# Kernel tuning notes

Hardware: AMD Instinct MI355X
Metric: run time of the kernel (lower is better)

The kernel has to match this reference:

```python
import jax, jax.numpy as jnp
import numpy as np

S, E, K = 100000, 30000, 1000
D, F = 64, 128
B = 16384
NNZ_S, NNZ_E, NNZ_K = 1600000, 480000, 32000
LAYERS = 3
MOMENTUM = 0.9
LEAK = 0.1


def setup_inputs() -> dict:
    key = jax.random.key(0)
    ks = jax.random.split(key, 24)
    inp = {}
    inp['student_id'] = jax.random.randint(ks[0], (B,), 0, S, dtype=jnp.int32)
    inp['exercise_id'] = jax.random.randint(ks[1], (B,), 0, E, dtype=jnp.int32)
    inp['q_mask'] = jnp.ones((B, K), jnp.float32)
    # embedding tables (xavier-ish scale)
    inp['stu_emb'] = jax.random.normal(ks[2], (S, D), jnp.float32) * 0.05
    inp['exer_emb'] = jax.random.normal(ks[3], (E, D), jnp.float32) * 0.05
    inp['know_emb'] = jax.random.normal(ks[4], (K, D), jnp.float32) * 0.05
    inp['impact_emb'] = jax.random.normal(ks[5], (E, D), jnp.float32) * 0.05
    # sparse adjacencies in COO form (rows, cols, vals); vals ~ normalized weights
    inp['s_rows'] = jax.random.randint(ks[6], (NNZ_S,), 0, S, dtype=jnp.int32)
    inp['s_cols'] = jax.random.randint(ks[7], (NNZ_S,), 0, S, dtype=jnp.int32)
    inp['s_vals'] = jax.random.uniform(ks[8], (NNZ_S,), jnp.float32) / 16.0
    inp['e_rows'] = jax.random.randint(ks[9], (NNZ_E,), 0, E, dtype=jnp.int32)
    inp['e_cols'] = jax.random.randint(ks[10], (NNZ_E,), 0, E, dtype=jnp.int32)
    inp['e_vals'] = jax.random.uniform(ks[11], (NNZ_E,), jnp.float32) / 16.0
    inp['k_rows'] = jax.random.randint(ks[12], (NNZ_K,), 0, K, dtype=jnp.int32)
    inp['k_cols'] = jax.random.randint(ks[13], (NNZ_K,), 0, K, dtype=jnp.int32)
    inp['k_vals'] = jax.random.uniform(ks[14], (NNZ_K,), jnp.float32) / 32.0
    # linear layers (stored as [in, out])
    inp['W_stu'] = jax.random.normal(ks[15], (D, F), jnp.float32) * 0.1
    inp['b_stu'] = jnp.zeros((F,), jnp.float32)
    inp['W_exer'] = jax.random.normal(ks[16], (D, F), jnp.float32) * 0.1
    inp['b_exer'] = jnp.zeros((F,), jnp.float32)
    inp['W_know'] = jax.random.normal(ks[17], (D, F), jnp.float32) * 0.1
    inp['b_know'] = jnp.zeros((F,), jnp.float32)
    inp['W_disc'] = jax.random.normal(ks[18], (D, 1), jnp.float32) * 0.1
    inp['b_disc'] = jnp.zeros((1,), jnp.float32)
    return inp


def spmm(rows, cols, vals, x, n):
    # sparse [n,n] @ dense [n,d] via gather + segment_sum
    return jax.ops.segment_sum(vals[:, None] * x[cols], rows, num_segments=n)


def convolution(emb, rows, cols, vals, n):
    # layers of SpMM with momentum residual; mean over all (layers+1) outputs
    acc = emb
    cur = emb
    for _ in range(LAYERS):
        cur = spmm(rows, cols, vals, cur, n) + MOMENTUM * cur
        acc = acc + cur
    return acc / (LAYERS + 1)


def reference(student_id, exercise_id, q_mask, stu_emb, exer_emb, know_emb,
              impact_emb, s_rows, s_cols, s_vals, e_rows, e_cols, e_vals,
              k_rows, k_cols, k_vals, W_stu, b_stu, W_exer, b_exer,
              W_know, b_know, W_disc, b_disc):
    stu_fwd = convolution(stu_emb, s_rows, s_cols, s_vals, S)    # [S, D]
    exer_fwd = convolution(exer_emb, e_rows, e_cols, e_vals, E)  # [E, D]
    know_fwd = convolution(know_emb, k_rows, k_cols, k_vals, K)  # [K, D]

    batch_student = stu_fwd[student_id]    # [B, D]
    batch_exercise = exer_fwd[exercise_id]  # [B, D]

    student_ts = jax.nn.leaky_relu(batch_student @ W_stu + b_stu, LEAK)   # [B, F]
    diff_ts = jax.nn.leaky_relu(batch_exercise @ W_exer + b_exer, LEAK)  # [B, F]
    knowledge_ts = jax.nn.leaky_relu(know_fwd @ W_know + b_know, LEAK)   # [K, F]
    disc_ts = jax.nn.sigmoid(batch_exercise @ W_disc + b_disc)          # [B, 1]

    student_ts = student_ts @ knowledge_ts.T  # [B, K]
    diff_ts = diff_ts @ knowledge_ts.T        # [B, K]
    knowledge_impact_ts = impact_emb[exercise_id]  # [B, D]
    return (student_ts, diff_ts, disc_ts, knowledge_ts, knowledge_impact_ts)
```

## Files before the change

### kernel.cpp

```cpp
#include <hip/hip_runtime.h>
#include <hip/hip_bf16.h>

#define S_N 100000
#define E_N 30000
#define K_N 1000
#define D_K 64
#define F_K 128
#define B_N 16384
#define NNZ_S 1600000
#define NNZ_E 480000
#define NNZ_K 32000
#define NNZ_TOT (NNZ_S + NNZ_E + NNZ_K)

#define CH_S 49
#define CH_E 15
#define CH_K 1
#define CH_TOT (CH_S + CH_E + CH_K)

#define NB_S 782
#define NB_E 235
#define NB_K 8
#define NB_TOT (NB_S + NB_E + NB_K)

#define CHUNK 4096
#define SB_S 391
#define SB_E 118
#define SB_K 8
#define SB_TOT (SB_S + SB_E + SB_K)

typedef __attribute__((ext_vector_type(8))) short sh8;
typedef __attribute__((ext_vector_type(4))) float f4;

__device__ inline float b2f(ushort u) { return __uint_as_float((unsigned)u << 16); }
__device__ inline ushort f2b(float f) {
    unsigned u = __float_as_uint(f);
    return (ushort)((u + 0x7fffu + ((u >> 16) & 1u)) >> 16);
}

__global__ void count_kernel(const int* __restrict__ sr, const int* __restrict__ er,
                             const int* __restrict__ kr,
                             int* cnt_s, int* cnt_e, int* cnt_k) {
    int i = blockIdx.x * 256 + threadIdx.x;
    if (i >= NNZ_TOT) return;
    if (i < NNZ_S) atomicAdd(&cnt_s[sr[i]], 1);
    else if (i < NNZ_S + NNZ_E) atomicAdd(&cnt_e[er[i - NNZ_S]], 1);
    else atomicAdd(&cnt_k[kr[i - NNZ_S - NNZ_E]], 1);
}

__device__ inline void seg_map(int b, const int* cnt_s, const int* cnt_e, const int* cnt_k,
                               const int** src, int* len, int* chunk, int* seg) {
    if (b < CH_S)            { *src = cnt_s; *len = S_N; *chunk = b;            *seg = 0; }
    else if (b < CH_S + CH_E){ *src = cnt_e; *len = E_N; *chunk = b - CH_S;     *seg = 1; }
    else                     { *src = cnt_k; *len = K_N; *chunk = 0;            *seg = 2; }
}

__global__ void scan_a(const int* cnt_s, const int* cnt_e, const int* cnt_k, int* partials) {
    const int* src; int len, chunk, seg;
    seg_map(blockIdx.x, cnt_s, cnt_e, cnt_k, &src, &len, &chunk, &seg);
    int base = chunk * 2048 + threadIdx.x * 8;
    int s = 0;
    for (int j = 0; j < 8; j++) { int idx = base + j; if (idx < len) s += src[idx]; }
    __shared__ int red[256];
    red[threadIdx.x] = s; __syncthreads();
    for (int off = 128; off > 0; off >>= 1) {
        if (threadIdx.x < off) red[threadIdx.x] += red[threadIdx.x + off];
        __syncthreads();
    }
    if (threadIdx.x == 0) partials[blockIdx.x] = red[0];
}

__global__ void scan_b(const int* partials, int* chunk_off, int* rp_s, int* rp_e, int* rp_k) {
    if (threadIdx.x == 0 && blockIdx.x == 0) {
        int acc = 0;
        for (int i = 0; i < CH_S; i++) { chunk_off[i] = acc; acc += partials[i]; }
        rp_s[S_N] = acc;
        acc = 0;
        for (int i = CH_S; i < CH_S + CH_E; i++) { chunk_off[i] = acc; acc += partials[i]; }
        rp_e[E_N] = acc;
        chunk_off[CH_S + CH_E] = 0;
        rp_k[K_N] = partials[CH_S + CH_E];
    }
}

__global__ void scan_c(const int* cnt_s, const int* cnt_e, const int* cnt_k,
                       const int* chunk_off,
                       int* rp_s, int* rp_e, int* rp_k) {
    const int* src; int len, chunk, seg;
    seg_map(blockIdx.x, cnt_s, cnt_e, cnt_k, &src, &len, &chunk, &seg);
    int* rp = (seg == 0) ? rp_s : (seg == 1) ? rp_e : rp_k;
    int t = threadIdx.x;
    int base = chunk * 2048 + t * 8;
    int v[8]; int s = 0;
    for (int j = 0; j < 8; j++) { int idx = base + j; v[j] = (idx < len) ? src[idx] : 0; s += v[j]; }
    __shared__ int sd[256];
    sd[t] = s; __syncthreads();
    for (int off = 1; off < 256; off <<= 1) {
        int x = (t >= off) ? sd[t - off] : 0;
        __syncthreads();
        sd[t] += x;
        __syncthreads();
    }
    int pre = sd[t] - s + chunk_off[blockIdx.x];
    for (int j = 0; j < 8; j++) {
        int idx = base + j;
        if (idx < len) { rp[idx] = pre; pre += v[j]; }
    }
}

__global__ void stage1_bin(const int* __restrict__ sr, const int* __restrict__ sc,
                           const float* __restrict__ sv,
                           const int* __restrict__ er, const int* __restrict__ ec,
                           const float* __restrict__ ev,
                           const int* __restrict__ kr, const int* __restrict__ kc,
                           const float* __restrict__ kv,
                           const int* __restrict__ rp_s, const int* __restrict__ rp_e,
                           const int* __restrict__ rp_k,
                           int* bcnt, int2* stg_s, int2* stg_e, int2* stg_k) {
    int blk = blockIdx.x;
    const int* rows; const int* cols; const float* vals; const int* rp;
    int2* stg; int boff, nnz, nb, lblk;
    if (blk < SB_S) {
        lblk = blk; rows = sr; cols = sc; vals = sv; rp = rp_s; stg = stg_s;
        boff = 0; nnz = NNZ_S; nb = NB_S;
    } else if (blk < SB_S + SB_E) {
        lblk = blk - SB_S; rows = er; cols = ec; vals = ev; rp = rp_e; stg = stg_e;
        boff = NB_S; nnz = NNZ_E; nb = NB_E;
    } else {
        lblk = blk - SB_S - SB_E; rows = kr; cols = kc; vals = kv; rp = rp_k; stg = stg_k;
        boff = NB_S + NB_E; nnz = NNZ_K; nb = NB_K;
    }
    __shared__ int hist[NB_S];
    __shared__ int wbase[NB_S];
    int t = threadIdx.x;
    for (int i = t; i < nb; i += 256) hist[i] = 0;
    __syncthreads();
    int start = lblk * CHUNK, end = min(start + CHUNK, nnz);
    for (int i = start + t; i < end; i += 256) atomicAdd(&hist[rows[i] >> 7], 1);
    __syncthreads();
    for (int i = t; i < nb; i += 256) {
        int h = hist[i];
        int b0 = h ? atomicAdd(&bcnt[boff + i], h) : 0;
        wbase[i] = rp[i << 7] + b0;
        hist[i] = 0;
    }
    __syncthreads();
    for (int i = start + t; i < end; i += 256) {
        int r = rows[i]; int b = r >> 7;
        int p = wbase[b] + atomicAdd(&hist[b], 1);
        stg[p] = make_int2(((r & 127) << 25) | cols[i], __float_as_int(vals[i]));
    }
}

__global__ void stage2_place(const int* __restrict__ rp_s, const int2* __restrict__ stg_s,
                             int2* pr_s,
                             const int* __restrict__ rp_e, const int2* __restrict__ stg_e,
                             int2* pr_e,
                             const int* __restrict__ rp_k, const int2* __restrict__ stg_k,
                             int2* pr_k) {
    int b = blockIdx.x;
    const int* rp; const int2* stg; int2* pr; int len;
    if (b < NB_S) { rp = rp_s; stg = stg_s; pr = pr_s; len = S_N; }
    else if (b < NB_S + NB_E) { b -= NB_S; rp = rp_e; stg = stg_e; pr = pr_e; len = E_N; }
    else { b -= NB_S + NB_E; rp = rp_k; stg = stg_k; pr = pr_k; len = K_N; }
    int r0 = b << 7;
    int rows = min(128, len - r0);
    __shared__ int nx[128];
    int t = threadIdx.x;
    if (t < rows) nx[t] = rp[r0 + t];
    __syncthreads();
    int j0 = rp[r0], j1 = rp[r0 + rows];
    for (int j = j0 + t; j < j1; j += 256) {
        int2 e = stg[j];
        int r_rel = ((unsigned)e.x) >> 25;
        int col = e.x & 0x01FFFFFF;
        int p = atomicAdd(&nx[r_rel], 1);
        pr[p] = make_int2(col, e.y);
    }
}

__global__ void convert_bf16(const float* __restrict__ a, const float* __restrict__ b,
                             const float* __restrict__ c,
                             ushort* oa, ushort* ob, ushort* oc) {
    const int NA = S_N * 64, NB = E_N * 64, NC = K_N * 64;
    int i = (blockIdx.x * 256 + threadIdx.x) * 4;
    const float* src; ushort* dst;
    if (i < NA) { src = a; dst = oa; }
    else if (i < NA + NB) { i -= NA; src = b; dst = ob; }
    else if (i < NA + NB + NC) { i -= NA + NB; src = c; dst = oc; }
    else return;
    float4 v = *(const float4*)&src[i];
    ushort4 o;
    o.x = f2b(v.x); o.y = f2b(v.y); o.z = f2b(v.z); o.w = f2b(v.w);
    *(ushort4*)&dst[i] = o;
}

__device__ __forceinline__ void spmm_row_compute(
        const int* __restrict__ rp, const int2* __restrict__ pr,
        const ushort* __restrict__ x, int r, int l, float* a) {
    const ushort4* __restrict__ X4 = (const ushort4*)x;
    int j0 = rp[r], j1 = rp[r + 1];
    ushort4 self = X4[r * 16 + l];
    float a0 = 0.9f * b2f(self.x), a1 = 0.9f * b2f(self.y);
    float a2 = 0.9f * b2f(self.z), a3 = 0.9f * b2f(self.w);
    int j = j0;
    for (; j + 8 <= j1; j += 8) {
        int2 q0 = pr[j + 0], q1 = pr[j + 1], q2 = pr[j + 2], q3 = pr[j + 3];
        int2 q4 = pr[j + 4], q5 = pr[j + 5], q6 = pr[j + 6], q7 = pr[j + 7];
        ushort4 v0 = X4[q0.x * 16 + l];
        ushort4 v1 = X4[q1.x * 16 + l];
        ushort4 v2 = X4[q2.x * 16 + l];
        ushort4 v3 = X4[q3.x * 16 + l];
        ushort4 v4 = X4[q4.x * 16 + l];
        ushort4 v5 = X4[q5.x * 16 + l];
        ushort4 v6 = X4[q6.x * 16 + l];
        ushort4 v7 = X4[q7.x * 16 + l];
        float w0 = __int_as_float(q0.y), w1 = __int_as_float(q1.y);
        float w2 = __int_as_float(q2.y), w3 = __int_as_float(q3.y);
        float w4 = __int_as_float(q4.y), w5 = __int_as_float(q5.y);
        float w6 = __int_as_float(q6.y), w7 = __int_as_float(q7.y);
        a0 = fmaf(w0, b2f(v0.x), a0); a1 = fmaf(w0, b2f(v0.y), a1);
        a2 = fmaf(w0, b2f(v0.z), a2); a3 = fmaf(w0, b2f(v0.w), a3);
        a0 = fmaf(w1, b2f(v1.x), a0); a1 = fmaf(w1, b2f(v1.y), a1);
        a2 = fmaf(w1, b2f(v1.z), a2); a3 = fmaf(w1, b2f(v1.w), a3);
        a0 = fmaf(w2, b2f(v2.x), a0); a1 = fmaf(w2, b2f(v2.y), a1);
        a2 = fmaf(w2, b2f(v2.z), a2); a3 = fmaf(w2, b2f(v2.w), a3);
        a0 = fmaf(w3, b2f(v3.x), a0); a1 = fmaf(w3, b2f(v3.y), a1);
        a2 = fmaf(w3, b2f(v3.z), a2); a3 = fmaf(w3, b2f(v3.w), a3);
        a0 = fmaf(w4, b2f(v4.x), a0); a1 = fmaf(w4, b2f(v4.y), a1);
        a2 = fmaf(w4, b2f(v4.z), a2); a3 = fmaf(w4, b2f(v4.w), a3);
        a0 = fmaf(w5, b2f(v5.x), a0); a1 = fmaf(w5, b2f(v5.y), a1);
        a2 = fmaf(w5, b2f(v5.z), a2); a3 = fmaf(w5, b2f(v5.w), a3);
        a0 = fmaf(w6, b2f(v6.x), a0); a1 = fmaf(w6, b2f(v6.y), a1);
        a2 = fmaf(w6, b2f(v6.z), a2); a3 = fmaf(w6, b2f(v6.w), a3);
        a0 = fmaf(w7, b2f(v7.x), a0); a1 = fmaf(w7, b2f(v7.y), a1);
        a2 = fmaf(w7, b2f(v7.z), a2); a3 = fmaf(w7, b2f(v7.w), a3);
    }
    if (j + 4 <= j1) {
        int2 q0 = pr[j + 0], q1 = pr[j + 1], q2 = pr[j + 2], q3 = pr[j + 3];
        ushort4 v0 = X4[q0.x * 16 + l];
        ushort4 v1 = X4[q1.x * 16 + l];
        ushort4 v2 = X4[q2.x * 16 + l];
        ushort4 v3 = X4[q3.x * 16 + l];
        float w0 = __int_as_float(q0.y), w1 = __int_as_float(q1.y);
        float w2 = __int_as_float(q2.y), w3 = __int_as_float(q3.y);
        a0 = fmaf(w0, b2f(v0.x), a0); a1 = fmaf(w0, b2f(v0.y), a1);
        a2 = fmaf(w0, b2f(v0.z), a2); a3 = fmaf(w0, b2f(v0.w), a3);
        a0 = fmaf(w1, b2f(v1.x), a0); a1 = fmaf(w1, b2f(v1.y), a1);
        a2 = fmaf(w1, b2f(v1.z), a2); a3 = fmaf(w1, b2f(v1.w), a3);
        a0 = fmaf(w2, b2f(v2.x), a0); a1 = fmaf(w2, b2f(v2.y), a1);
        a2 = fmaf(w2, b2f(v2.z), a2); a3 = fmaf(w2, b2f(v2.w), a3);
        a0 = fmaf(w3, b2f(v3.x), a0); a1 = fmaf(w3, b2f(v3.y), a1);
        a2 = fmaf(w3, b2f(v3.z), a2); a3 = fmaf(w3, b2f(v3.w), a3);
        j += 4;
    }
    if (j < j1) {
        int last = j1 - 1;
        int2 q0 = pr[j];
        int2 q1 = pr[min(j + 1, last)];
        int2 q2 = pr[min(j + 2, last)];
        int2 q3 = pr[min(j + 3, last)];
        ushort4 v0 = X4[q0.x * 16 + l];
        ushort4 v1 = X4[q1.x * 16 + l];
        ushort4 v2 = X4[q2.x * 16 + l];
        ushort4 v3 = X4[q3.x * 16 + l];
        float w0 = __int_as_float(q0.y);
        float w1 = (j + 1 <= last) ? __int_as_float(q1.y) : 0.f;
        float w2 = (j + 2 <= last) ? __int_as_float(q2.y) : 0.f;
        float w3 = (j + 3 <= last) ? __int_as_float(q3.y) : 0.f;
        a0 = fmaf(w0, b2f(v0.x), a0); a1 = fmaf(w0, b2f(v0.y), a1);
        a2 = fmaf(w0, b2f(v0.z), a2); a3 = fmaf(w0, b2f(v0.w), a3);
        a0 = fmaf(w1, b2f(v1.x), a0); a1 = fmaf(w1, b2f(v1.y), a1);
        a2 = fmaf(w1, b2f(v1.z), a2); a3 = fmaf(w1, b2f(v1.w), a3);
        a0 = fmaf(w2, b2f(v2.x), a0); a1 = fmaf(w2, b2f(v2.y), a1);
        a2 = fmaf(w2, b2f(v2.z), a2); a3 = fmaf(w2, b2f(v2.w), a3);
        a0 = fmaf(w3, b2f(v3.x), a0); a1 = fmaf(w3, b2f(v3.y), a1);
        a2 = fmaf(w3, b2f(v3.z), a2); a3 = fmaf(w3, b2f(v3.w), a3);
    }
    a[0] = a0; a[1] = a1; a[2] = a2; a[3] = a3;
}

__global__ void spmm_full(const int* __restrict__ rp_s, const int2* __restrict__ pr_s,
                          const ushort* __restrict__ xs, ushort* ys,
                          const int* __restrict__ rp_e, const int2* __restrict__ pr_e,
                          const ushort* __restrict__ xe, ushort* ye,
                          const int* __restrict__ rp_k, const int2* __restrict__ pr_k,
                          const ushort* __restrict__ xk, ushort* yk) {
    int w = (blockIdx.x * 256 + threadIdx.x) >> 4;
    int l = threadIdx.x & 15;
    const int* rp; const int2* pr; const ushort* x; ushort* y; int r;
    if (w < S_N) { rp = rp_s; pr = pr_s; x = xs; y = ys; r = w; }
    else if (w < S_N + E_N) { rp = rp_e; pr = pr_e; x = xe; y = ye; r = w - S_N; }
    else if (w < S_N + E_N + K_N) { rp = rp_k; pr = pr_k; x = xk; y = yk; r = w - S_N - E_N; }
    else return;
    float a[4];
    spmm_row_compute(rp, pr, x, r, l, a);
    ushort4 o;
    o.x = f2b(a[0]); o.y = f2b(a[1]); o.z = f2b(a[2]); o.w = f2b(a[3]);
    *(ushort4*)&y[r * 64 + l * 4] = o;
}

__global__ void spmm_last(const int* __restrict__ sid, const int* __restrict__ eid,
                          const int* __restrict__ rp_s, const int2* __restrict__ pr_s,
                          const ushort* __restrict__ xs, ushort* c3s,
                          const int* __restrict__ rp_e, const int2* __restrict__ pr_e,
                          const ushort* __restrict__ xe, ushort* c3e,
                          const int* __restrict__ rp_k, const int2* __restrict__ pr_k,
                          const ushort* __restrict__ xk, ushort* yk) {
    int w = (blockIdx.x * 256 + threadIdx.x) >> 4;
    int l = threadIdx.x & 15;
    const int* rp; const int2* pr; const ushort* x; ushort* y; int r; int orow;
    if (w < B_N) { rp = rp_s; pr = pr_s; x = xs; y = c3s; r = sid[w]; orow = w; }
    else if (w < 2 * B_N) {
        int b = w - B_N;
        rp = rp_e; pr = pr_e; x = xe; y = c3e; r = eid[b]; orow = b;
    } else if (w < 2 * B_N + K_N) {
        r = w - 2 * B_N;
        rp = rp_k; pr = pr_k; x = xk; y = yk; orow = r;
    } else return;
    float a[4];
    spmm_row_compute(rp, pr, x, r, l, a);
    ushort4 o;
    o.x = f2b(a[0]); o.y = f2b(a[1]); o.z = f2b(a[2]); o.w = f2b(a[3]);
    *(ushort4*)&y[orow * 64 + l * 4] = o;
}

__global__ void gather_init(const int* __restrict__ sid, const int* __restrict__ eid,
                            const float* __restrict__ src_s, const float* __restrict__ src_e,
                            const float* __restrict__ src_k,
                            float* bacc_s, float* bacc_e, float* kacc) {
    int i = blockIdx.x * 256 + threadIdx.x;
    const int BD = B_N * 64;
    if (i < BD) {
        int b = i >> 6, d = i & 63;
        bacc_s[i] = src_s[(long)sid[b] * 64 + d];
    } else if (i < 2 * BD) {
        int ii = i - BD; int b = ii >> 6, d = ii & 63;
        bacc_e[ii] = src_e[(long)eid[b] * 64 + d];
    } else if (i < 2 * BD + K_N * 64) {
        int ii = i - 2 * BD;
        kacc[ii] = src_k[ii];
    }
}

__global__ void gather_accb(const int* __restrict__ sid, const int* __restrict__ eid,
                            const ushort* __restrict__ src_s, const ushort* __restrict__ src_e,
                            const ushort* __restrict__ src_k,
                            float* bacc_s, float* bacc_e, float* kacc) {
    int i = blockIdx.x * 256 + threadIdx.x;
    const int BD = B_N * 64;
    if (i < BD) {
        int b = i >> 6, d = i & 63;
        bacc_s[i] += b2f(src_s[(long)sid[b] * 64 + d]);
    } else if (i < 2 * BD) {
        int ii = i - BD; int b = ii >> 6, d = ii & 63;
        bacc_e[ii] += b2f(src_e[(long)eid[b] * 64 + d]);
    } else if (i < 2 * BD + K_N * 64) {
        int ii = i - 2 * BD;
        kacc[ii] += b2f(src_k[ii]);
    }
}

__global__ void dense_mm(const float* __restrict__ bacc_s, const ushort* __restrict__ c3_s,
                         const float* __restrict__ bacc_e, const ushort* __restrict__ c3_e,
                         const float* __restrict__ W_stu, const float* __restrict__ b_stu,
                         const float* __restrict__ W_exer, const float* __restrict__ b_exer,
                         __hip_bfloat16* st_b, __hip_bfloat16* df_b) {
    int which = blockIdx.y;
    const float* bacc = which ? bacc_e : bacc_s;
    const ushort* c3 = which ? c3_e : c3_s;
    const float* W = which ? W_exer : W_stu;
    const float* bias = which ? b_exer : b_stu;
    __hip_bfloat16* out = which ? df_b : st_b;
    int r0 = blockIdx.x * 2;
    int t = threadIdx.x;
    __shared__ float X[2][64];
    if (t < 128) {
        int lr = t >> 6, d = t & 63; int b = r0 + lr;
        X[lr][d] = 0.25f * (bacc[(long)b * 64 + d] + b2f(c3[(long)b * 64 + d]));
    }
    __syncthreads();
    int lr = t >> 7, f = t & 127;
    float acc = bias[f];
    for (int d = 0; d < 64; d++) acc += X[lr][d] * W[d * 128 + f];
    acc = acc > 0.f ? acc : 0.1f * acc;
    out[(long)(r0 + lr) * 128 + f] = __float2bfloat16(acc);
}

__global__ void know_mm(const float* __restrict__ kacc, const ushort* __restrict__ cur3_k,
                        const float* __restrict__ W, const float* __restrict__ bias,
                        float* out_f32, __hip_bfloat16* kn_b) {
    int r0 = blockIdx.x * 2;
    int t = threadIdx.x;
    __shared__ float X[2][64];
    if (t < 128) {
        int lr = t >> 6, d = t & 63; int r = r0 + lr;
        X[lr][d] = (r < K_N) ? 0.25f * (kacc[r * 64 + d] + b2f(cur3_k[r * 64 + d])) : 0.f;
    }
    __syncthreads();
    int lr = t >> 7, f = t & 127; int r = r0 + lr;
    float acc = bias[f];
    for (int d = 0; d < 64; d++) acc += X[lr][d] * W[d * 128 + f];
    acc = acc > 0.f ? acc : 0.1f * acc;
    if (r < K_N) {
        out_f32[(long)r * 128 + f] = acc;
        kn_b[(long)r * 128 + f] = __float2bfloat16(acc);
    } else {
        kn_b[(long)r * 128 + f] = __float2bfloat16(0.f);
    }
}

__global__ void disc_kernel(const float* __restrict__ bacc_e, const ushort* __restrict__ c3_e,
                            const float* __restrict__ W_disc, const float* __restrict__ b_disc,
                            float* out) {
    int w = (blockIdx.x * 256 + threadIdx.x) >> 6;
    int d = threadIdx.x & 63;
    if (w >= B_N) return;
    float x = 0.25f * (bacc_e[(long)w * 64 + d] + b2f(c3_e[(long)w * 64 + d])) * W_disc[d];
    for (int off = 32; off > 0; off >>= 1) x += __shfl_down(x, off, 64);
    if (d == 0) {
        float z = x + b_disc[0];
        out[w] = 1.f / (1.f + expf(-z));
    }
}

__global__ void impact_kernel(const int* __restrict__ eid, const float* __restrict__ imp,
                              float* out) {
    int i = blockIdx.x * 256 + threadIdx.x;
    if (i >= B_N * 64) return;
    int b = i >> 6, d = i & 63;
    out[i] = imp[(long)eid[b] * 64 + d];
}

__global__ void big_mm(const __hip_bfloat16* __restrict__ st, const __hip_bfloat16* __restrict__ df,
                       const __hip_bfloat16* __restrict__ kn,
                       float* __restrict__ out0, float* __restrict__ out1) {
    const ushort* X = (const ushort*)(blockIdx.z ? df : st);
    const ushort* Kn = (const ushort*)kn;
    float* out = blockIdx.z ? out1 : out0;
    int wv = threadIdx.x >> 6;
    int lane = threadIdx.x & 63;
    int m_blk = blockIdx.y * 64 + (wv >> 1) * 32;
    int n_blk = blockIdx.x * 64 + (wv & 1) * 32;
    int q = lane >> 4, l16 = lane & 15;
    f4 acc00 = {0.f, 0.f, 0.f, 0.f}, acc01 = acc00, acc10 = acc00, acc11 = acc00;
    for (int s = 0; s < 4; s++) {
        int kofs = s * 32 + q * 8;
        sh8 a0 = *(const sh8*)&X[(long)(m_blk + l16) * 128 + kofs];
        sh8 a1 = *(const sh8*)&X[(long)(m_blk + 16 + l16) * 128 + kofs];
        sh8 b0 = *(const sh8*)&Kn[(long)(n_blk + l16) * 128 + kofs];
        sh8 b1 = *(const sh8*)&Kn[(long)(n_blk + 16 + l16) * 128 + kofs];
        acc00 = __builtin_amdgcn_mfma_f32_16x16x32_bf16(a0, b0, acc00, 0, 0, 0);
        acc01 = __builtin_amdgcn_mfma_f32_16x16x32_bf16(a0, b1, acc01, 0, 0, 0);
        acc10 = __builtin_amdgcn_mfma_f32_16x16x32_bf16(a1, b0, acc10, 0, 0, 0);
        acc11 = __builtin_amdgcn_mfma_f32_16x16x32_bf16(a1, b1, acc11, 0, 0, 0);
    }
    for (int r = 0; r < 4; r++) {
        int row0 = m_blk + q * 4 + r;
        int row1 = m_blk + 16 + q * 4 + r;
        int col0 = n_blk + l16;
        int col1 = n_blk + 16 + l16;
        if (col0 < K_N) {
            out[(long)row0 * K_N + col0] = acc00[r];
            out[(long)row1 * K_N + col0] = acc10[r];
        }
        if (col1 < K_N) {
            out[(long)row0 * K_N + col1] = acc01[r];
            out[(long)row1 * K_N + col1] = acc11[r];
        }
    }
}

extern "C" void kernel_launch(void* const* d_in, const int* in_sizes, int n_in,
                              void* d_out, int out_size, void* d_ws, size_t ws_size,
                              hipStream_t stream) {
    const int* sid = (const int*)d_in[0];
    const int* eid = (const int*)d_in[1];
    const float* stu_emb = (const float*)d_in[3];
    const float* exer_emb = (const float*)d_in[4];
    const float* know_emb = (const float*)d_in[5];
    const float* impact_emb = (const float*)d_in[6];
    const int* s_rows = (const int*)d_in[7];
    const int* s_cols = (const int*)d_in[8];
    const float* s_vals = (const float*)d_in[9];
    const int* e_rows = (const int*)d_in[10];
    const int* e_cols = (const int*)d_in[11];
    const float* e_vals = (const float*)d_in[12];
    const int* k_rows = (const int*)d_in[13];
    const int* k_cols = (const int*)d_in[14];
    const float* k_vals = (const float*)d_in[15];
    const float* W_stu = (const float*)d_in[16];
    const float* b_stu = (const float*)d_in[17];
    const float* W_exer = (const float*)d_in[18];
    const float* b_exer = (const float*)d_in[19];
    const float* W_know = (const float*)d_in[20];
    const float* b_know = (const float*)d_in[21];
    const float* W_disc = (const float*)d_in[22];
    const float* b_disc = (const float*)d_in[23];

    float* out = (float*)d_out;
    float* out_st = out;
    float* out_df = out + 16384000;
    float* out_disc = out + 32768000;
    float* out_kn = out + 32784384;
    float* out_imp = out + 32912384;

    char* p = (char*)d_ws;
    auto alloc = [&](size_t bytes) -> char* {
        char* r = p;
        p += (bytes + 255) & ~(size_t)255;
        return r;
    };
    ushort* xb_s = (ushort*)alloc((size_t)S_N * 64 * 2);
    ushort* xb_e = (ushort*)alloc((size_t)E_N * 64 * 2);
    ushort* xb_k = (ushort*)alloc((size_t)K_N * 64 * 2);
    ushort* bufA_s = (ushort*)alloc((size_t)S_N * 64 * 2);
    ushort* bufB_s = (ushort*)alloc((size_t)S_N * 64 * 2);
    ushort* bufA_e = (ushort*)alloc((size_t)E_N * 64 * 2);
    ushort* bufB_e = (ushort*)alloc((size_t)E_N * 64 * 2);
    ushort* bufA_k = (ushort*)alloc((size_t)K_N * 64 * 2);
    ushort* bufB_k = (ushort*)alloc((size_t)K_N * 64 * 2);
    ushort* c3s = (ushort*)alloc((size_t)B_N * 64 * 2);
    ushort* c3e = (ushort*)alloc((size_t)B_N * 64 * 2);
    float* bacc_s = (float*)alloc((size_t)B_N * 64 * 4);
    float* bacc_e = (float*)alloc((size_t)B_N * 64 * 4);
    float* kacc = (float*)alloc((size_t)K_N * 64 * 4);
    __hip_bfloat16* st_b = (__hip_bfloat16*)alloc((size_t)B_N * 128 * 2);
    __hip_bfloat16* df_b = (__hip_bfloat16*)alloc((size_t)B_N * 128 * 2);
    __hip_bfloat16* kn_b = (__hip_bfloat16*)alloc((size_t)1024 * 128 * 2);
    int* cnt_s = (int*)alloc((size_t)(S_N + E_N + K_N + NB_TOT) * 4);
    int* cnt_e = cnt_s + S_N;
    int* cnt_k = cnt_e + E_N;
    int* bcnt = cnt_k + K_N;
    int* rp_s = (int*)alloc((size_t)(S_N + 1) * 4);
    int* rp_e = (int*)alloc((size_t)(E_N + 1) * 4);
    int* rp_k = (int*)alloc((size_t)(K_N + 1) * 4);
    int2* stg_s = (int2*)alloc((size_t)NNZ_S * 8);
    int2* stg_e = (int2*)alloc((size_t)NNZ_E * 8);
    int2* stg_k = (int2*)alloc((size_t)NNZ_K * 8);
    int2* pr_s = (int2*)alloc((size_t)NNZ_S * 8);
    int2* pr_e = (int2*)alloc((size_t)NNZ_E * 8);
    int2* pr_k = (int2*)alloc((size_t)NNZ_K * 8);
    int* partials = (int*)alloc(CH_TOT * 4);
    int* chunk_off = (int*)alloc(CH_TOT * 4);

    hipMemsetAsync(cnt_s, 0, (size_t)(S_N + E_N + K_N + NB_TOT) * 4, stream);
    count_kernel<<<NNZ_TOT / 256, 256, 0, stream>>>(s_rows, e_rows, k_rows, cnt_s, cnt_e, cnt_k);
    scan_a<<<CH_TOT, 256, 0, stream>>>(cnt_s, cnt_e, cnt_k, partials);
    scan_b<<<1, 64, 0, stream>>>(partials, chunk_off, rp_s, rp_e, rp_k);
    scan_c<<<CH_TOT, 256, 0, stream>>>(cnt_s, cnt_e, cnt_k, chunk_off, rp_s, rp_e, rp_k);
    stage1_bin<<<SB_TOT, 256, 0, stream>>>(
        s_rows, s_cols, s_vals, e_rows, e_cols, e_vals, k_rows, k_cols, k_vals,
        rp_s, rp_e, rp_k, bcnt, stg_s, stg_e, stg_k);
    stage2_place<<<NB_TOT, 256, 0, stream>>>(rp_s, stg_s, pr_s,
                                             rp_e, stg_e, pr_e,
                                             rp_k, stg_k, pr_k);

    const int conv_blocks = ((S_N + E_N + K_N) * 64 / 4 + 255) / 256;
    convert_bf16<<<conv_blocks, 256, 0, stream>>>(stu_emb, exer_emb, know_emb, xb_s, xb_e, xb_k);

    const int gather_blocks = (2 * B_N * 64 + K_N * 64) / 256;
    const int full_blocks = ((S_N + E_N + K_N) * 16 + 255) / 256;
    const int last_blocks = ((2 * B_N + K_N) * 16 + 255) / 256;
    gather_init<<<gather_blocks, 256, 0, stream>>>(sid, eid, stu_emb, exer_emb, know_emb,
                                                   bacc_s, bacc_e, kacc);
    spmm_full<<<full_blocks, 256, 0, stream>>>(rp_s, pr_s, xb_s, bufA_s,
                                               rp_e, pr_e, xb_e, bufA_e,
                                               rp_k, pr_k, xb_k, bufA_k);
    gather_accb<<<gather_blocks, 256, 0, stream>>>(sid, eid, bufA_s, bufA_e, bufA_k,
                                                   bacc_s, bacc_e, kacc);
    spmm_full<<<full_blocks, 256, 0, stream>>>(rp_s, pr_s, bufA_s, bufB_s,
                                               rp_e, pr_e, bufA_e, bufB_e,
                                               rp_k, pr_k, bufA_k, bufB_k);
    gather_accb<<<gather_blocks, 256, 0, stream>>>(sid, eid, bufB_s, bufB_e, bufB_k,
                                                   bacc_s, bacc_e, kacc);
    spmm_last<<<last_blocks, 256, 0, stream>>>(sid, eid,
                                               rp_s, pr_s, bufB_s, c3s,
                                               rp_e, pr_e, bufB_e, c3e,
                                               rp_k, pr_k, bufB_k, bufA_k);

    dense_mm<<<dim3(B_N / 2, 2), 256, 0, stream>>>(bacc_s, c3s, bacc_e, c3e,
                                                   W_stu, b_stu, W_exer, b_exer, st_b, df_b);
    know_mm<<<512, 256, 0, stream>>>(kacc, bufA_k, W_know, b_know, out_kn, kn_b);
    disc_kernel<<<B_N / 4, 256, 0, stream>>>(bacc_e, c3e, W_disc, b_disc, out_disc);
    impact_kernel<<<B_N * 64 / 256, 256, 0, stream>>>(eid, impact_emb, out_imp);

    big_mm<<<dim3(16, B_N / 64, 2), 256, 0, stream>>>(st_b, df_b, kn_b, out_st, out_df);
}
```

Before: 656.8 us.

## Replace per-row count and scan with bucket-level histogram, derive row pointers in placement

```diff
diff --git a/kernel.cpp b/kernel.cpp
--- a/kernel.cpp
+++ b/kernel.cpp
@@ -12,11 +12,6 @@
 #define NNZ_K 32000
 #define NNZ_TOT (NNZ_S + NNZ_E + NNZ_K)
 
-#define CH_S 49
-#define CH_E 15
-#define CH_K 1
-#define CH_TOT (CH_S + CH_E + CH_K)
-
 #define NB_S 782
 #define NB_E 235
 #define NB_K 8
@@ -37,62 +32,36 @@
     return (ushort)((u + 0x7fffu + ((u >> 16) & 1u)) >> 16);
 }
 
-__global__ void count_kernel(const int* __restrict__ sr, const int* __restrict__ er,
-                             const int* __restrict__ kr,
-                             int* cnt_s, int* cnt_e, int* cnt_k) {
-    int i = blockIdx.x * 256 + threadIdx.x;
-    if (i >= NNZ_TOT) return;
-    if (i < NNZ_S) atomicAdd(&cnt_s[sr[i]], 1);
-    else if (i < NNZ_S + NNZ_E) atomicAdd(&cnt_e[er[i - NNZ_S]], 1);
-    else atomicAdd(&cnt_k[kr[i - NNZ_S - NNZ_E]], 1);
-}
-
-__device__ inline void seg_map(int b, const int* cnt_s, const int* cnt_e, const int* cnt_k,
-                               const int** src, int* len, int* chunk, int* seg) {
-    if (b < CH_S)            { *src = cnt_s; *len = S_N; *chunk = b;            *seg = 0; }
-    else if (b < CH_S + CH_E){ *src = cnt_e; *len = E_N; *chunk = b - CH_S;     *seg = 1; }
-    else                     { *src = cnt_k; *len = K_N; *chunk = 0;            *seg = 2; }
-}
-
-__global__ void scan_a(const int* cnt_s, const int* cnt_e, const int* cnt_k, int* partials) {
-    const int* src; int len, chunk, seg;
-    seg_map(blockIdx.x, cnt_s, cnt_e, cnt_k, &src, &len, &chunk, &seg);
-    int base = chunk * 2048 + threadIdx.x * 8;
-    int s = 0;
-    for (int j = 0; j < 8; j++) { int idx = base + j; if (idx < len) s += src[idx]; }
-    __shared__ int red[256];
-    red[threadIdx.x] = s; __syncthreads();
-    for (int off = 128; off > 0; off >>= 1) {
-        if (threadIdx.x < off) red[threadIdx.x] += red[threadIdx.x + off];
-        __syncthreads();
-    }
-    if (threadIdx.x == 0) partials[blockIdx.x] = red[0];
-}
-
-__global__ void scan_b(const int* partials, int* chunk_off, int* rp_s, int* rp_e, int* rp_k) {
-    if (threadIdx.x == 0 && blockIdx.x == 0) {
-        int acc = 0;
-        for (int i = 0; i < CH_S; i++) { chunk_off[i] = acc; acc += partials[i]; }
-        rp_s[S_N] = acc;
-        acc = 0;
-        for (int i = CH_S; i < CH_S + CH_E; i++) { chunk_off[i] = acc; acc += partials[i]; }
-        rp_e[E_N] = acc;
-        chunk_off[CH_S + CH_E] = 0;
-        rp_k[K_N] = partials[CH_S + CH_E];
-    }
-}
-
-__global__ void scan_c(const int* cnt_s, const int* cnt_e, const int* cnt_k,
-                       const int* chunk_off,
-                       int* rp_s, int* rp_e, int* rp_k) {
-    const int* src; int len, chunk, seg;
-    seg_map(blockIdx.x, cnt_s, cnt_e, cnt_k, &src, &len, &chunk, &seg);
-    int* rp = (seg == 0) ? rp_s : (seg == 1) ? rp_e : rp_k;
+__global__ void bucket_count(const int* __restrict__ sr, const int* __restrict__ er,
+                             const int* __restrict__ kr, int* bcnt_tot) {
+    int blk = blockIdx.x;
+    const int* rows; int boff, nnz, nb, lblk;
+    if (blk < SB_S)            { lblk = blk;              rows = sr; boff = 0;           nnz = NNZ_S; nb = NB_S; }
+    else if (blk < SB_S + SB_E){ lblk = blk - SB_S;       rows = er; boff = NB_S;        nnz = NNZ_E; nb = NB_E; }
+    else                       { lblk = blk - SB_S - SB_E; rows = kr; boff = NB_S + NB_E; nnz = NNZ_K; nb = NB_K; }
+    __shared__ int hist[NB_S];
     int t = threadIdx.x;
-    int base = chunk * 2048 + t * 8;
-    int v[8]; int s = 0;
-    for (int j = 0; j < 8; j++) { int idx = base + j; v[j] = (idx < len) ? src[idx] : 0; s += v[j]; }
+    for (int i = t; i < nb; i += 256) hist[i] = 0;
+    __syncthreads();
+    int start = lblk * CHUNK, end = min(start + CHUNK, nnz);
+    for (int i = start + t; i < end; i += 256) atomicAdd(&hist[rows[i] >> 7], 1);
+    __syncthreads();
+    for (int i = t; i < nb; i += 256) {
+        int h = hist[i];
+        if (h) atomicAdd(&bcnt_tot[boff + i], h);
+    }
+}
+
+__global__ void bucket_scan(const int* __restrict__ bcnt_tot, int* bucket_base,
+                            int* rp_s, int* rp_e, int* rp_k) {
     __shared__ int sd[256];
+    int t = threadIdx.x;
+    int v[5]; int s = 0;
+    for (int j = 0; j < 5; j++) {
+        int idx = t * 5 + j;
+        v[j] = (idx < NB_TOT) ? bcnt_tot[idx] : 0;
+        s += v[j];
+    }
     sd[t] = s; __syncthreads();
     for (int off = 1; off < 256; off <<= 1) {
         int x = (t >= off) ? sd[t - off] : 0;
@@ -100,11 +69,16 @@
         sd[t] += x;
         __syncthreads();
     }
-    int pre = sd[t] - s + chunk_off[blockIdx.x];
-    for (int j = 0; j < 8; j++) {
-        int idx = base + j;
-        if (idx < len) { rp[idx] = pre; pre += v[j]; }
-    }
+    int pre = sd[t] - s;
+    for (int j = 0; j < 5; j++) {
+        int idx = t * 5 + j;
+        if (idx < NB_TOT) {
+            int segoff = (idx < NB_S) ? 0 : (idx < NB_S + NB_E) ? NNZ_S : (NNZ_S + NNZ_E);
+            bucket_base[idx] = pre - segoff;
+            pre += v[j];
+        }
+    }
+    if (t == 0) { rp_s[S_N] = NNZ_S; rp_e[E_N] = NNZ_E; rp_k[K_N] = NNZ_K; }
 }
 
 __global__ void stage1_bin(const int* __restrict__ sr, const int* __restrict__ sc,
@@ -113,20 +87,19 @@
                            const float* __restrict__ ev,
                            const int* __restrict__ kr, const int* __restrict__ kc,
                            const float* __restrict__ kv,
-                           const int* __restrict__ rp_s, const int* __restrict__ rp_e,
-                           const int* __restrict__ rp_k,
-                           int* bcnt, int2* stg_s, int2* stg_e, int2* stg_k) {
+                           const int* __restrict__ bucket_base,
+                           int* rsv, int2* stg_s, int2* stg_e, int2* stg_k) {
     int blk = blockIdx.x;
-    const int* rows; const int* cols; const float* vals; const int* rp;
+    const int* rows; const int* cols; const float* vals;
     int2* stg; int boff, nnz, nb, lblk;
     if (blk < SB_S) {
-        lblk = blk; rows = sr; cols = sc; vals = sv; rp = rp_s; stg = stg_s;
+        lblk = blk; rows = sr; cols = sc; vals = sv; stg = stg_s;
         boff = 0; nnz = NNZ_S; nb = NB_S;
     } else if (blk < SB_S + SB_E) {
-        lblk = blk - SB_S; rows = er; cols = ec; vals = ev; rp = rp_e; stg = stg_e;
+        lblk = blk - SB_S; rows = er; cols = ec; vals = ev; stg = stg_e;
         boff = NB_S; nnz = NNZ_E; nb = NB_E;
     } else {
-        lblk = blk - SB_S - SB_E; rows = kr; cols = kc; vals = kv; rp = rp_k; stg = stg_k;
+        lblk = blk - SB_S - SB_E; rows = kr; cols = kc; vals = kv; stg = stg_k;
         boff = NB_S + NB_E; nnz = NNZ_K; nb = NB_K;
     }
     __shared__ int hist[NB_S];
@@ -139,8 +112,8 @@
     __syncthreads();
     for (int i = t; i < nb; i += 256) {
         int h = hist[i];
-        int b0 = h ? atomicAdd(&bcnt[boff + i], h) : 0;
-        wbase[i] = rp[i << 7] + b0;
+        int b0 = h ? atomicAdd(&rsv[boff + i], h) : 0;
+        wbase[i] = bucket_base[boff + i] + b0;
         hist[i] = 0;
     }
     __syncthreads();
@@ -151,24 +124,40 @@
     }
 }
 
-__global__ void stage2_place(const int* __restrict__ rp_s, const int2* __restrict__ stg_s,
-                             int2* pr_s,
-                             const int* __restrict__ rp_e, const int2* __restrict__ stg_e,
-                             int2* pr_e,
-                             const int* __restrict__ rp_k, const int2* __restrict__ stg_k,
-                             int2* pr_k) {
-    int b = blockIdx.x;
-    const int* rp; const int2* stg; int2* pr; int len;
-    if (b < NB_S) { rp = rp_s; stg = stg_s; pr = pr_s; len = S_N; }
-    else if (b < NB_S + NB_E) { b -= NB_S; rp = rp_e; stg = stg_e; pr = pr_e; len = E_N; }
-    else { b -= NB_S + NB_E; rp = rp_k; stg = stg_k; pr = pr_k; len = K_N; }
+__global__ void stage2_place(const int* __restrict__ bucket_base, const int* __restrict__ bcnt_tot,
+                             const int2* __restrict__ stg_s, int2* pr_s, int* rp_s,
+                             const int2* __restrict__ stg_e, int2* pr_e, int* rp_e,
+                             const int2* __restrict__ stg_k, int2* pr_k, int* rp_k) {
+    int gb = blockIdx.x;
+    int b = gb;
+    const int2* stg; int2* pr; int* rp; int len;
+    if (b < NB_S) { stg = stg_s; pr = pr_s; rp = rp_s; len = S_N; }
+    else if (b < NB_S + NB_E) { b -= NB_S; stg = stg_e; pr = pr_e; rp = rp_e; len = E_N; }
+    else { b -= NB_S + NB_E; stg = stg_k; pr = pr_k; rp = rp_k; len = K_N; }
     int r0 = b << 7;
     int rows = min(128, len - r0);
+    __shared__ int cnt[128];
     __shared__ int nx[128];
     int t = threadIdx.x;
-    if (t < rows) nx[t] = rp[r0 + t];
-    __syncthreads();
-    int j0 = rp[r0], j1 = rp[r0 + rows];
+    if (t < 128) cnt[t] = 0;
+    __syncthreads();
+    int j0 = bucket_base[gb], j1 = j0 + bcnt_tot[gb];
+    for (int j = j0 + t; j < j1; j += 256)
+        atomicAdd(&cnt[((unsigned)stg[j].x) >> 25], 1);
+    __syncthreads();
+    int my = (t < 128) ? cnt[t] : 0;
+    for (int off = 1; off < 128; off <<= 1) {
+        int y = (t < 128 && t >= off) ? cnt[t - off] : 0;
+        __syncthreads();
+        if (t < 128) cnt[t] += y;
+        __syncthreads();
+    }
+    if (t < 128) {
+        int ex = j0 + cnt[t] - my;
+        nx[t] = ex;
+        if (t < rows) rp[r0 + t] = ex;
+    }
+    __syncthreads();
     for (int j = j0 + t; j < j1; j += 256) {
         int2 e = stg[j];
         int r_rel = ((unsigned)e.x) >> 25;
@@ -527,10 +516,9 @@
     __hip_bfloat16* st_b = (__hip_bfloat16*)alloc((size_t)B_N * 128 * 2);
     __hip_bfloat16* df_b = (__hip_bfloat16*)alloc((size_t)B_N * 128 * 2);
     __hip_bfloat16* kn_b = (__hip_bfloat16*)alloc((size_t)1024 * 128 * 2);
-    int* cnt_s = (int*)alloc((size_t)(S_N + E_N + K_N + NB_TOT) * 4);
-    int* cnt_e = cnt_s + S_N;
-    int* cnt_k = cnt_e + E_N;
-    int* bcnt = cnt_k + K_N;
+    int* bcnt_tot = (int*)alloc((size_t)2 * NB_TOT * 4);
+    int* rsv = bcnt_tot + NB_TOT;
+    int* bucket_base = (int*)alloc((size_t)NB_TOT * 4);
     int* rp_s = (int*)alloc((size_t)(S_N + 1) * 4);
     int* rp_e = (int*)alloc((size_t)(E_N + 1) * 4);
     int* rp_k = (int*)alloc((size_t)(K_N + 1) * 4);
@@ -540,20 +528,17 @@
     int2* pr_s = (int2*)alloc((size_t)NNZ_S * 8);
     int2* pr_e = (int2*)alloc((size_t)NNZ_E * 8);
     int2* pr_k = (int2*)alloc((size_t)NNZ_K * 8);
-    int* partials = (int*)alloc(CH_TOT * 4);
-    int* chunk_off = (int*)alloc(CH_TOT * 4);
-
-    hipMemsetAsync(cnt_s, 0, (size_t)(S_N + E_N + K_N + NB_TOT) * 4, stream);
-    count_kernel<<<NNZ_TOT / 256, 256, 0, stream>>>(s_rows, e_rows, k_rows, cnt_s, cnt_e, cnt_k);
-    scan_a<<<CH_TOT, 256, 0, stream>>>(cnt_s, cnt_e, cnt_k, partials);
-    scan_b<<<1, 64, 0, stream>>>(partials, chunk_off, rp_s, rp_e, rp_k);
-    scan_c<<<CH_TOT, 256, 0, stream>>>(cnt_s, cnt_e, cnt_k, chunk_off, rp_s, rp_e, rp_k);
+
+    hipMemsetAsync(bcnt_tot, 0, (size_t)2 * NB_TOT * 4, stream);
+    bucket_count<<<SB_TOT, 256, 0, stream>>>(s_rows, e_rows, k_rows, bcnt_tot);
+    bucket_scan<<<1, 256, 0, stream>>>(bcnt_tot, bucket_base, rp_s, rp_e, rp_k);
     stage1_bin<<<SB_TOT, 256, 0, stream>>>(
         s_rows, s_cols, s_vals, e_rows, e_cols, e_vals, k_rows, k_cols, k_vals,
-        rp_s, rp_e, rp_k, bcnt, stg_s, stg_e, stg_k);
-    stage2_place<<<NB_TOT, 256, 0, stream>>>(rp_s, stg_s, pr_s,
-                                             rp_e, stg_e, pr_e,
-                                             rp_k, stg_k, pr_k);
+        bucket_base, rsv, stg_s, stg_e, stg_k);
+    stage2_place<<<NB_TOT, 256, 0, stream>>>(bucket_base, bcnt_tot,
+                                             stg_s, pr_s, rp_s,
+                                             stg_e, pr_e, rp_e,
+                                             stg_k, pr_k, rp_k);
 
     const int conv_blocks = ((S_N + E_N + K_N) * 64 / 4 + 255) / 256;
     convert_bf16<<<conv_blocks, 256, 0, stream>>>(stu_emb, exer_emb, know_emb, xb_s, xb_e, xb_k);
```

New measurement: 570.6 us. 13.1% less time.
